# Kernel optimization log

Hardware: AMD Instinct MI355X
Metric: run time of the kernel (lower is better)

The kernel has to match this reference:

```python
import jax, jax.numpy as jnp
import numpy as np

DIM = 96
HEADS = 3
RES = (128, 128)
KH, KW = 8, 8
SH, SW = 4, 4  # window_size // 2, shift enabled
N = KH * KW
EPS_LN = 1e-5


def _rel_tables():
    # relative coords table fed to CPB-MLP, shape [(2KH-1)*(2KW-1), 2]
    ch = np.arange(-(KH - 1), KH, dtype=np.float32)
    cw = np.arange(-(KW - 1), KW, dtype=np.float32)
    t = np.stack(np.meshgrid(ch, cw, indexing='ij'), axis=-1)
    t[..., 0] /= (KH - 1)
    t[..., 1] /= (KW - 1)
    t *= 8.0
    t = np.sign(t) * np.log2(np.abs(t) + 1.0) / np.log2(8.0)
    # relative position index, shape [N, N]
    coords = np.stack(np.meshgrid(np.arange(KH), np.arange(KW), indexing='ij'))
    cf = coords.reshape(2, -1)
    rel = (cf[:, :, None] - cf[:, None, :]).transpose(1, 2, 0)
    rel[..., 0] += KH - 1
    rel[..., 1] += KW - 1
    rel[..., 0] *= 2 * KW - 1
    idx = rel.sum(-1)
    return jnp.asarray(t.reshape(-1, 2)), jnp.asarray(idx)


def _attn_mask():
    # shifted-window attention mask, shape [nW, N, N]
    H, W = RES
    img = np.zeros((H, W), np.float32)
    cnt = 0
    for hs in (slice(0, -KH), slice(-KH, -SH), slice(-SH, None)):
        for ws in (slice(0, -KW), slice(-KW, -SW), slice(-SW, None)):
            img[hs, ws] = cnt
            cnt += 1
    mw = img.reshape(H // KH, KH, W // KW, KW).transpose(0, 2, 1, 3).reshape(-1, N)
    am = mw[:, None, :] - mw[:, :, None]
    am = np.where(am != 0, -100.0, 0.0).astype(np.float32)
    return jnp.asarray(am)


_CPB_TABLE, _REL_IDX = _rel_tables()
_ATTN_MASK = _attn_mask()


def _layernorm(x, w, b):
    mu = x.mean(-1, keepdims=True)
    var = x.var(-1, keepdims=True)
    return (x - mu) / jnp.sqrt(var + EPS_LN) * w + b


def setup_inputs() -> dict:
    key = jax.random.key(0)
    ks = jax.random.split(key, 16)
    B = 32
    H, W = RES
    hid = 4 * DIM
    s = 0.02
    return {
        'x': jax.random.normal(ks[0], (B, H * W, DIM), jnp.float32),
        'norm1_w': jnp.ones((DIM,), jnp.float32),
        'norm1_b': jnp.zeros((DIM,), jnp.float32),
        'qkv_w': jax.random.normal(ks[1], (3 * DIM, DIM), jnp.float32) * s,
        'q_bias': jnp.zeros((DIM,), jnp.float32),
        'v_bias': jnp.zeros((DIM,), jnp.float32),
        'logit_scale': jnp.full((HEADS, 1, 1), np.log(10.0), jnp.float32),
        'cpb_w1': jax.random.normal(ks[2], (512, 2), jnp.float32) * s,
        'cpb_b1': jnp.zeros((512,), jnp.float32),
        'cpb_w2': jax.random.normal(ks[3], (HEADS, 512), jnp.float32) * s,
        'proj_w': jax.random.normal(ks[4], (DIM, DIM), jnp.float32) * s,
        'proj_b': jnp.zeros((DIM,), jnp.float32),
        'norm2_w': jnp.ones((DIM,), jnp.float32),
        'norm2_b': jnp.zeros((DIM,), jnp.float32),
        'mlp_w1': jax.random.normal(ks[5], (hid, DIM), jnp.float32) * s,
        'mlp_b1': jnp.zeros((hid,), jnp.float32),
        'mlp_w2': jax.random.normal(ks[6], (DIM, hid), jnp.float32) * s,
        'mlp_b2': jnp.zeros((DIM,), jnp.float32),
    }


def reference(x, norm1_w, norm1_b, qkv_w, q_bias, v_bias, logit_scale,
              cpb_w1, cpb_b1, cpb_w2, proj_w, proj_b,
              norm2_w, norm2_b, mlp_w1, mlp_b1, mlp_w2, mlp_b2):
    B, L, C = x.shape
    H, W = RES
    hd = C // HEADS
    shortcut = x

    # cyclic shift + window partition: [B*nW, N, C]
    xi = jnp.roll(x.reshape(B, H, W, C), (-SH, -SW), axis=(1, 2))
    xw = xi.reshape(B, H // KH, KH, W // KW, KW, C).transpose(0, 1, 3, 2, 4, 5)
    xw = xw.reshape(-1, N, C)
    B_ = xw.shape[0]

    # qkv with zero k-bias
    qkv_b = jnp.concatenate([q_bias, jnp.zeros_like(v_bias), v_bias])
    qkv = (xw @ qkv_w.T + qkv_b).reshape(B_, N, 3, HEADS, hd).transpose(2, 0, 3, 1, 4)
    q, k, v = qkv[0], qkv[1], qkv[2]

    # cosine attention with clamped learned logit scale
    qn = q / jnp.maximum(jnp.linalg.norm(q, axis=-1, keepdims=True), 1e-12)
    kn = k / jnp.maximum(jnp.linalg.norm(k, axis=-1, keepdims=True), 1e-12)
    attn = jnp.einsum('bhnd,bhmd->bhnm', qn, kn)
    ls = jnp.exp(jnp.minimum(logit_scale, jnp.log(100.0)))
    attn = attn * ls

    # CPB-MLP relative position bias, gathered into [heads, N, N]
    bias_t = jax.nn.relu(_CPB_TABLE @ cpb_w1.T + cpb_b1) @ cpb_w2.T
    rpb = 16.0 * jax.nn.sigmoid(bias_t[_REL_IDX]).transpose(2, 0, 1)
    attn = attn + rpb[None]

    # shift mask, then softmax
    nW = _ATTN_MASK.shape[0]
    attn = attn.reshape(B_ // nW, nW, HEADS, N, N) + _ATTN_MASK[None, :, None]
    attn = jax.nn.softmax(attn.reshape(B_, HEADS, N, N), axis=-1)

    out = jnp.einsum('bhnm,bhmd->bhnd', attn, v).transpose(0, 2, 1, 3).reshape(B_, N, C)
    out = out @ proj_w.T + proj_b

    # window reverse + reverse shift
    out = out.reshape(B, H // KH, W // KW, KH, KW, C).transpose(0, 1, 3, 2, 4, 5)
    out = out.reshape(B, H, W, C)
    out = jnp.roll(out, (SH, SW), axis=(1, 2)).reshape(B, L, C)

    # SwinV2 post-norm residuals
    x = shortcut + _layernorm(out, norm1_w, norm1_b)
    h = jax.nn.gelu(x @ mlp_w1.T + mlp_b1, approximate=False) @ mlp_w2.T + mlp_b2
    x = x + _layernorm(h, norm2_w, norm2_b)
    return x
```

## Files before the change

kernel.cpp:

```cpp
#include <hip/hip_runtime.h>
#include <math.h>


constexpr int WIN=8, CD=96, RH=128, RW=128, SHF=4;

constexpr int KN_S=40, VT_S=72, WB_S=104;
constexpr int OFF_KN=0;
constexpr int OFF_VT=2560;
constexpr int PAN_SH=10240;
constexpr int OFF_WB0=4864;
constexpr int OFF_WB1=15104;
constexpr int LDS_SHORTS=25344;
constexpr int LDS_BYTES = LDS_SHORTS*2;

typedef float f32x4 __attribute__((ext_vector_type(4)));
typedef short s16x8 __attribute__((ext_vector_type(8)));
typedef short s16x4 __attribute__((ext_vector_type(4)));
typedef int   i32x2 __attribute__((ext_vector_type(2)));
typedef int   i32x4 __attribute__((ext_vector_type(4)));
typedef unsigned int u32x2 __attribute__((ext_vector_type(2)));

#define MFMA16(a,b,c) __builtin_amdgcn_mfma_f32_16x16x32_bf16((a),(b),(c),0,0,0)

#if __has_builtin(__builtin_amdgcn_permlane32_swap) && __has_builtin(__builtin_amdgcn_permlane16_swap)
#define HAVE_PLSWAP 1
#else
#define HAVE_PLSWAP 0
#endif

#define RAW_LDS_BARRIER() do { \
    asm volatile("s_waitcnt lgkmcnt(0)" ::: "memory"); \
    __builtin_amdgcn_s_barrier(); \
    asm volatile("" ::: "memory"); } while (0)

__device__ __forceinline__ short f2bf(float f) {
    __bf16 b = (__bf16)f;
    return __builtin_bit_cast(short, b);
}
__device__ __forceinline__ s16x8 ld8(const short* p) {
    return *reinterpret_cast<const s16x8*>(p);
}
__device__ __forceinline__ s16x4 pack4(float a, float b, float c, float d) {
    s16x4 r; r[0]=f2bf(a); r[1]=f2bf(b); r[2]=f2bf(c); r[3]=f2bf(d);
    return r;
}
__device__ __forceinline__ s16x8 abf_from_f32(const float* p) {
    const f32x4* q = reinterpret_cast<const f32x4*>(p);
    f32x4 a = q[0], b = q[1];
    s16x8 r;
    r[0]=f2bf(a[0]); r[1]=f2bf(a[1]); r[2]=f2bf(a[2]); r[3]=f2bf(a[3]);
    r[4]=f2bf(b[0]); r[5]=f2bf(b[1]); r[6]=f2bf(b[2]); r[7]=f2bf(b[3]);
    return r;
}

#if HAVE_PLSWAP
__device__ __forceinline__ void plswap32(unsigned &a, unsigned &b) {
    u32x2 r = __builtin_amdgcn_permlane32_swap(a, b, false, false);
    a = r[0]; b = r[1];
}
__device__ __forceinline__ void plswap16(unsigned &a, unsigned &b) {
    u32x2 r = __builtin_amdgcn_permlane16_swap(a, b, false, false);
    a = r[0]; b = r[1];
}
#endif

__device__ __forceinline__ s16x8 xposeT(s16x4 p0, s16x4 p1, int l) {
    i32x2 q0 = __builtin_bit_cast(i32x2, p0);
    i32x2 q1 = __builtin_bit_cast(i32x2, p1);
#if HAVE_PLSWAP
    (void)l;
    unsigned a0 = (unsigned)q0[0], a1 = (unsigned)q0[1];
    unsigned b0 = (unsigned)q1[0], b1 = (unsigned)q1[1];
    plswap32(a0, b0);
    plswap32(a1, b1);
    plswap16(a0, b0);
    plswap16(a1, b1);
    i32x4 w; w[0]=(int)a0; w[1]=(int)a1; w[2]=(int)b0; w[3]=(int)b1;
    return __builtin_bit_cast(s16x8, w);
#else
    const int l15 = l & 15, lg = l >> 4;
    const int L1 = l15 + (((2*lg  )&3)<<4);
    const int L2 = l15 + (((2*lg+1)&3)<<4);
    const bool lo = (lg & 2) == 0;
    int a0 = __shfl(q0[0], L1), b0 = __shfl(q1[0], L1);
    int a1 = __shfl(q0[1], L1), b1 = __shfl(q1[1], L1);
    int a2 = __shfl(q0[0], L2), b2 = __shfl(q1[0], L2);
    int a3 = __shfl(q0[1], L2), b3 = __shfl(q1[1], L2);
    i32x4 w;
    w[0] = lo ? a0 : b0;
    w[1] = lo ? a1 : b1;
    w[2] = lo ? a2 : b2;
    w[3] = lo ? a3 : b3;
    return __builtin_bit_cast(s16x8, w);
#endif
}
__device__ __forceinline__ float xsum4(float v) {
#if HAVE_PLSWAP
    unsigned a = __builtin_bit_cast(unsigned, v), b = a;
    plswap16(a, b);
    float s = __builtin_bit_cast(float, a) + __builtin_bit_cast(float, b);
    unsigned c = __builtin_bit_cast(unsigned, s), d = c;
    plswap32(c, d);
    return __builtin_bit_cast(float, c) + __builtin_bit_cast(float, d);
#else
    v += __shfl_xor(v,16); v += __shfl_xor(v,32); return v;
#endif
}
__device__ __forceinline__ float xmax4(float v) {
#if HAVE_PLSWAP
    unsigned a = __builtin_bit_cast(unsigned, v), b = a;
    plswap16(a, b);
    float s = fmaxf(__builtin_bit_cast(float, a), __builtin_bit_cast(float, b));
    unsigned c = __builtin_bit_cast(unsigned, s), d = c;
    plswap32(c, d);
    return fmaxf(__builtin_bit_cast(float, c), __builtin_bit_cast(float, d));
#else
    v = fmaxf(v, __shfl_xor(v,16)); v = fmaxf(v, __shfl_xor(v,32)); return v;
#endif
}
__device__ __forceinline__ int region_id(int hh, int ww) {
    int rr = (hh < RH-WIN) ? 0 : ((hh < RH-SHF) ? 1 : 2);
    int rc = (ww < RW-WIN) ? 0 : ((ww < RW-SHF) ? 1 : 2);
    return rr*3 + rc;
}
__device__ __forceinline__ float gelu_f(float h) {
    float u = h * (1.5957691216f + 0.0713548163f * h * h);
    float e = __expf(-u);
    return h * __builtin_amdgcn_rcpf(1.f + e);
}

__device__ __forceinline__ void stage_panel(const short* __restrict__ pan,
                                            short* dst, int wv, int l) {
    const char* g = (const char*)pan + l*16;
    char* d = (char*)dst;
    #pragma unroll
    for (int k = 0; k < 5; ++k) {
        int i = wv + k*4;
        __builtin_amdgcn_global_load_lds(
            (const __attribute__((address_space(1))) unsigned int*)(g + i*1024),
            (__attribute__((address_space(3))) unsigned int*)(d + i*1024),
            16, 0, 0);
    }
}

__global__ __launch_bounds__(256) void cpb_kernel(
    const float* __restrict__ w1, const float* __restrict__ b1,
    const float* __restrict__ w2, float* __restrict__ rpb)
{
    int g = blockIdx.x*256 + threadIdx.x;
    if (g >= 225*3) return;
    int e = g/3, h = g - e*3;
    int a = e/15, bb = e - a*15;
    float z0 = (float)(a-7) * (8.0f/7.0f);
    float z1 = (float)(bb-7) * (8.0f/7.0f);
    float s0 = (z0>0.f)?1.f:((z0<0.f)?-1.f:0.f);
    float s1 = (z1>0.f)?1.f:((z1<0.f)?-1.f:0.f);
    float t0 = s0 * log2f(fabsf(z0)+1.f) * (1.f/3.f);
    float t1 = s1 * log2f(fabsf(z1)+1.f) * (1.f/3.f);
    float acc = 0.f;
    for (int k = 0; k < 512; ++k) {
        float hv = t0*w1[2*k] + t1*w1[2*k+1] + b1[k];
        hv = fmaxf(hv, 0.f);
        acc += hv * w2[h*512 + k];
    }
    rpb[g] = 16.f / (1.f + __expf(-acc));
}

__global__ __launch_bounds__(256) void biasbuild_kernel(
    const float* __restrict__ rpb, float* __restrict__ biasT)
{
    int g = blockIdx.x*256 + threadIdx.x;
    if (g >= 3*64*64) return;
    int h = g >> 12, rem = g & 4095, i = rem >> 6, j = rem & 63;
    int ih = i>>3, iw = i&7, jh = j>>3, jw = j&7;
    int idx = (ih-jh+7)*15 + (iw-jw+7);
    biasT[g] = rpb[idx*3 + h];
}

__global__ __launch_bounds__(256) void wcvt_kernel(
    const float* __restrict__ qkvw, const float* __restrict__ projw,
    const float* __restrict__ w1,   const float* __restrict__ w2,
    short* __restrict__ wpan)
{
    int i = blockIdx.x*256 + threadIdx.x;
    if (i >= 12*9216) return;
    int p = i / 9216;
    int rem = i - p*9216;
    int r = rem / 96;
    int col = rem - r*96;
    float v;
    if (p < 3)        v = qkvw[((r>>5)*96 + p*32 + (r&31))*96 + col];
    else if (p == 3)  v = projw[r*96 + col];
    else if (((p-4)&1) == 0) { int c = (p-4)>>1; v = w1[(c*96 + r)*96 + col]; }
    else              { int c = (p-4)>>1; v = w2[r*384 + c*96 + col]; }
    wpan[p*PAN_SH + r*WB_S + col] = f2bf(v);
}

__global__ __launch_bounds__(256,3) void fused_kernel(
    const float* __restrict__ x,
    const float* __restrict__ n1w, const float* __restrict__ n1b,
    const float* __restrict__ qb,  const float* __restrict__ vb,
    const float* __restrict__ lgs, const float* __restrict__ pb,
    const float* __restrict__ n2w, const float* __restrict__ n2b,
    const float* __restrict__ b1,  const float* __restrict__ b2,
    const float* __restrict__ biasT,
    const short* __restrict__ wpan,
    float* __restrict__ out)
{
    extern __shared__ __align__(16) short smem[];
    short* kn  = smem + OFF_KN;
    short* vt  = smem + OFF_VT;
    short* wb0 = smem + OFF_WB0;
    short* wb1 = smem + OFF_WB1;

    const int t = threadIdx.x;
    const int l = t & 63;
    const int wv = t >> 6;
    const int l15 = l & 15;
    const int lg  = l >> 4;

    const int wid = blockIdx.x;
    const int b = wid >> 8, wi = wid & 255, wh = wi >> 4, ww = wi & 15;
    const float* xb = x + (size_t)b * (RH*RW*CD);

    const int arow = wv*16 + l15;
    const int ahs = (wh*WIN + (arow>>3) + SHF) & (RH-1);
    const int aws = (ww*WIN + (arow&7)  + SHF) & (RW-1);
    const unsigned go = ((unsigned)(b << 14) + ahs*RW + aws) * CD;
    const float* xrow = xb + (ahs*RW + aws)*CD;
    s16x8 xa[3];
    #pragma unroll
    for (int kt = 0; kt < 3; ++kt) xa[kt] = abf_from_f32(xrow + kt*32 + lg*8);

    f32x4 maskv[4];
    {
        int regi = region_id(wh*WIN + (arow>>3), ww*WIN + (arow&7));
        #pragma unroll
        for (int mt = 0; mt < 4; ++mt)
            #pragma unroll
            for (int rr = 0; rr < 4; ++rr) {
                int j = mt*16 + lg*4 + rr;
                int regj = region_id(wh*WIN + (j>>3), ww*WIN + (j&7));
                maskv[mt][rr] = (regi != regj) ? -100.f : 0.f;
            }
    }

    stage_panel(wpan, wb0, wv, l);

    s16x4 aop[6];

    #pragma unroll
    for (int h = 0; h < 3; ++h) {
        __syncthreads();
        stage_panel(wpan + (h+1)*PAN_SH, (h&1) ? wb0 : wb1, wv, l);
        const short* wbuf = (h&1) ? wb1 : wb0;

        const float ls = __expf(fminf(lgs[h], 4.60517019f));

        f32x4 qbf[2], vbf[2];
        #pragma unroll
        for (int nt = 0; nt < 2; ++nt) {
            qbf[nt] = *reinterpret_cast<const f32x4*>(qb + h*32 + nt*16 + lg*4);
            vbf[nt] = *reinterpret_cast<const f32x4*>(vb + h*32 + nt*16 + lg*4);
        }

        f32x4 qc[2], kc[2], vc[2];
        #pragma unroll
        for (int sec = 0; sec < 3; ++sec) {
            #pragma unroll
            for (int nt = 0; nt < 2; ++nt) {
                f32x4 c = (sec==0) ? qbf[nt]
                        : (sec==2) ? vbf[nt] : (f32x4){0.f,0.f,0.f,0.f};
                const short* wp = wbuf + (sec*32 + nt*16 + l15)*WB_S;
                #pragma unroll
                for (int kt = 0; kt < 3; ++kt)
                    c = MFMA16(ld8(wp + kt*32 + lg*8), xa[kt], c);
                if (sec==0) qc[nt]=c; else if (sec==1) kc[nt]=c; else vc[nt]=c;
            }
        }
        float sq = ((qc[0][0]*qc[0][0] + qc[0][1]*qc[0][1])
                  + (qc[0][2]*qc[0][2] + qc[0][3]*qc[0][3]))
                 + ((qc[1][0]*qc[1][0] + qc[1][1]*qc[1][1])
                  + (qc[1][2]*qc[1][2] + qc[1][3]*qc[1][3]));
        float sk = ((kc[0][0]*kc[0][0] + kc[0][1]*kc[0][1])
                  + (kc[0][2]*kc[0][2] + kc[0][3]*kc[0][3]))
                 + ((kc[1][0]*kc[1][0] + kc[1][1]*kc[1][1])
                  + (kc[1][2]*kc[1][2] + kc[1][3]*kc[1][3]));
        sq = xsum4(sq);
        sk = xsum4(sk);
        float scq = ls * __builtin_amdgcn_rsqf(fmaxf(sq, 1e-24f));
        float sck =      __builtin_amdgcn_rsqf(fmaxf(sk, 1e-24f));

        s16x4 qp0 = pack4(qc[0][0]*scq, qc[0][1]*scq, qc[0][2]*scq, qc[0][3]*scq);
        s16x4 qp1 = pack4(qc[1][0]*scq, qc[1][1]*scq, qc[1][2]*scq, qc[1][3]*scq);
        #pragma unroll
        for (int nt = 0; nt < 2; ++nt) {
            *reinterpret_cast<s16x4*>(kn + arow*KN_S + nt*16 + lg*4) =
                pack4(kc[nt][0]*sck, kc[nt][1]*sck, kc[nt][2]*sck, kc[nt][3]*sck);
            #pragma unroll
            for (int rr = 0; rr < 4; ++rr)
                vt[(nt*16 + lg*4 + rr)*VT_S + arow] = f2bf(vc[nt][rr]);
        }
        RAW_LDS_BARRIER();

        f32x4 bvm[4];
        const float* bh = biasT + h*4096 + arow*64;
        #pragma unroll
        for (int mt = 0; mt < 4; ++mt) {
            f32x4 bv = *reinterpret_cast<const f32x4*>(bh + mt*16 + lg*4);
            #pragma unroll
            for (int rr = 0; rr < 4; ++rr) bvm[mt][rr] = bv[rr] + maskv[mt][rr];
        }

        s16x8 qA = xposeT(qp0, qp1, l);
        f32x4 st[4];
        #pragma unroll
        for (int mt = 0; mt < 4; ++mt)
            st[mt] = MFMA16(ld8(kn + (mt*16 + l15)*KN_S + lg*8), qA, bvm[mt]);

        float m0 = fmaxf(fmaxf(st[0][0],st[0][1]), fmaxf(st[0][2],st[0][3]));
        float m1 = fmaxf(fmaxf(st[1][0],st[1][1]), fmaxf(st[1][2],st[1][3]));
        float m2 = fmaxf(fmaxf(st[2][0],st[2][1]), fmaxf(st[2][2],st[2][3]));
        float m3 = fmaxf(fmaxf(st[3][0],st[3][1]), fmaxf(st[3][2],st[3][3]));
        float mx = xmax4(fmaxf(fmaxf(m0,m1), fmaxf(m2,m3)));
        float sp[4];
        #pragma unroll
        for (int mt = 0; mt < 4; ++mt) {
            #pragma unroll
            for (int rr = 0; rr < 4; ++rr)
                st[mt][rr] = __expf(st[mt][rr] - mx);
            sp[mt] = (st[mt][0] + st[mt][1]) + (st[mt][2] + st[mt][3]);
        }
        float sm = xsum4((sp[0] + sp[1]) + (sp[2] + sp[3]));
        float inv = __builtin_amdgcn_rcpf(sm);

        s16x4 pw[4];
        #pragma unroll
        for (int mt = 0; mt < 4; ++mt)
            pw[mt] = pack4(st[mt][0], st[mt][1], st[mt][2], st[mt][3]);

        s16x8 pB0 = xposeT(pw[0], pw[1], l);
        s16x8 pB1 = xposeT(pw[2], pw[3], l);
        #pragma unroll
        for (int nt2 = 0; nt2 < 2; ++nt2) {
            f32x4 o = {0.f,0.f,0.f,0.f};
            o = MFMA16(ld8(vt + (nt2*16+l15)*VT_S + 0  + lg*8), pB0, o);
            o = MFMA16(ld8(vt + (nt2*16+l15)*VT_S + 32 + lg*8), pB1, o);
            aop[h*2 + nt2] = pack4(o[0]*inv, o[1]*inv, o[2]*inv, o[3]*inv);
        }
    }

    stage_panel(wpan + 4*PAN_SH, wb0, wv, l);

    s16x8 aB[3];
    #pragma unroll
    for (int kt = 0; kt < 3; ++kt)
        aB[kt] = xposeT(aop[2*kt], aop[2*kt+1], l);
    f32x4 pc[6];
    #pragma unroll
    for (int nt = 0; nt < 6; ++nt) {
        f32x4 c = *reinterpret_cast<const f32x4*>(pb + nt*16 + lg*4);
        const short* wp = wb1 + (nt*16 + l15)*WB_S;
        #pragma unroll
        for (int kt = 0; kt < 3; ++kt)
            c = MFMA16(ld8(wp + kt*32 + lg*8), aB[kt], c);
        pc[nt] = c;
    }

    f32x4 x1v[6];
    s16x4 x1p[6];
    {
        float sA=0.f, sB=0.f, s2A=0.f, s2B=0.f;
        #pragma unroll
        for (int nt = 0; nt < 6; ++nt) {
            f32x4 v = pc[nt];
            float ps  = (v[0]+v[1]) + (v[2]+v[3]);
            float ps2 = (v[0]*v[0]+v[1]*v[1]) + (v[2]*v[2]+v[3]*v[3]);
            if (nt & 1) { sB += ps; s2B += ps2; } else { sA += ps; s2A += ps2; }
        }
        float s = xsum4(sA + sB), s2 = xsum4(s2A + s2B);
        float mu  = s * (1.f/96.f);
        float var = s2 * (1.f/96.f) - mu*mu;
        float rstd = __builtin_amdgcn_rsqf(var + 1e-5f);
        #pragma unroll
        for (int nt = 0; nt < 6; ++nt) {
            f32x4 w1f = *reinterpret_cast<const f32x4*>(n1w + nt*16 + lg*4);
            f32x4 b1f = *reinterpret_cast<const f32x4*>(n1b + nt*16 + lg*4);
            f32x4 xv  = *reinterpret_cast<const f32x4*>(x + go + nt*16 + lg*4);
            f32x4 v;
            #pragma unroll
            for (int rr = 0; rr < 4; ++rr)
                v[rr] = xv[rr] + (pc[nt][rr] - mu)*rstd*w1f[rr] + b1f[rr];
            x1v[nt] = v;
            x1p[nt] = pack4(v[0], v[1], v[2], v[3]);
        }
    }

    s16x8 x1B[3];
    #pragma unroll
    for (int kt = 0; kt < 3; ++kt)
        x1B[kt] = xposeT(x1p[2*kt], x1p[2*kt+1], l);

    f32x4 oa[6];
    #pragma unroll
    for (int nt = 0; nt < 6; ++nt)
        oa[nt] = *reinterpret_cast<const f32x4*>(b2 + nt*16 + lg*4);

    for (int c = 0; c < 4; ++c) {
        __syncthreads();
        stage_panel(wpan + (5+2*c)*PAN_SH, wb1, wv, l);
        s16x4 hp[6];
        #pragma unroll
        for (int nt = 0; nt < 6; ++nt) {
            f32x4 a = *reinterpret_cast<const f32x4*>(b1 + c*96 + nt*16 + lg*4);
            const short* wp = wb0 + (nt*16 + l15)*WB_S;
            #pragma unroll
            for (int kt = 0; kt < 3; ++kt)
                a = MFMA16(ld8(wp + kt*32 + lg*8), x1B[kt], a);
            hp[nt] = pack4(gelu_f(a[0]), gelu_f(a[1]), gelu_f(a[2]), gelu_f(a[3]));
        }
        __syncthreads();
        if (c < 3) stage_panel(wpan + (6+2*c)*PAN_SH, wb0, wv, l);
        s16x8 hB[3];
        #pragma unroll
        for (int kt = 0; kt < 3; ++kt)
            hB[kt] = xposeT(hp[2*kt], hp[2*kt+1], l);
        #pragma unroll
        for (int nt = 0; nt < 6; ++nt) {
            const short* wp = wb1 + (nt*16 + l15)*WB_S;
            #pragma unroll
            for (int kt = 0; kt < 3; ++kt)
                oa[nt] = MFMA16(ld8(wp + kt*32 + lg*8), hB[kt], oa[nt]);
        }
    }

    {
        float sA=0.f, sB=0.f, s2A=0.f, s2B=0.f;
        #pragma unroll
        for (int nt = 0; nt < 6; ++nt) {
            f32x4 v = oa[nt];
            float ps  = (v[0]+v[1]) + (v[2]+v[3]);
            float ps2 = (v[0]*v[0]+v[1]*v[1]) + (v[2]*v[2]+v[3]*v[3]);
            if (nt & 1) { sB += ps; s2B += ps2; } else { sA += ps; s2A += ps2; }
        }
        float s = xsum4(sA + sB), s2 = xsum4(s2A + s2B);
        float mu  = s * (1.f/96.f);
        float var = s2 * (1.f/96.f) - mu*mu;
        float rstd = __builtin_amdgcn_rsqf(var + 1e-5f);
        #pragma unroll
        for (int nt = 0; nt < 6; ++nt) {
            f32x4 w2f = *reinterpret_cast<const f32x4*>(n2w + nt*16 + lg*4);
            f32x4 bb2 = *reinterpret_cast<const f32x4*>(n2b + nt*16 + lg*4);
            f32x4 res;
            #pragma unroll
            for (int rr = 0; rr < 4; ++rr)
                res[rr] = x1v[nt][rr] + (oa[nt][rr] - mu)*rstd*w2f[rr] + bb2[rr];
            *reinterpret_cast<f32x4*>(out + go + nt*16 + lg*4) = res;
        }
    }
}

extern "C" void kernel_launch(void* const* d_in, const int* in_sizes, int n_in,
                              void* d_out, int out_size, void* d_ws, size_t ws_size,
                              hipStream_t stream) {
    const float* x       = (const float*)d_in[0];
    const float* norm1_w = (const float*)d_in[1];
    const float* norm1_b = (const float*)d_in[2];
    const float* qkv_w   = (const float*)d_in[3];
    const float* q_bias  = (const float*)d_in[4];
    const float* v_bias  = (const float*)d_in[5];
    const float* lgs     = (const float*)d_in[6];
    const float* cpb_w1  = (const float*)d_in[7];
    const float* cpb_b1  = (const float*)d_in[8];
    const float* cpb_w2  = (const float*)d_in[9];
    const float* proj_w  = (const float*)d_in[10];
    const float* proj_b  = (const float*)d_in[11];
    const float* norm2_w = (const float*)d_in[12];
    const float* norm2_b = (const float*)d_in[13];
    const float* mlp_w1  = (const float*)d_in[14];
    const float* mlp_b1  = (const float*)d_in[15];
    const float* mlp_w2  = (const float*)d_in[16];
    const float* mlp_b2  = (const float*)d_in[17];

    char* wsb = (char*)d_ws;
    float* rpbTab = (float*)wsb;
    float* biasT  = (float*)(wsb + 4096);
    short* wpan   = (short*)(wsb + 53248);

    float* out = (float*)d_out;

    hipFuncSetAttribute(reinterpret_cast<const void*>(fused_kernel),
                        hipFuncAttributeMaxDynamicSharedMemorySize, LDS_BYTES);

    cpb_kernel<<<3, 256, 0, stream>>>(cpb_w1, cpb_b1, cpb_w2, rpbTab);
    biasbuild_kernel<<<48, 256, 0, stream>>>(rpbTab, biasT);
    wcvt_kernel<<<432, 256, 0, stream>>>(qkv_w, proj_w, mlp_w1, mlp_w2, wpan);
    fused_kernel<<<8192, 256, LDS_BYTES, stream>>>(x, norm1_w, norm1_b,
                                                   q_bias, v_bias, lgs, proj_b,
                                                   norm2_w, norm2_b, mlp_b1, mlp_b2,
                                                   biasT, wpan, out);
}
```

Measured before the change: 376.7 us.

## Software-pipeline next head's QKV projection under current head's softmax

Restructures the per-head attention loop so the QKV MFMA projection for head h+1 is issued right after the score MFMAs of head h. It then overlaps with that head's softmax and PV work. Both first weight panels are staged up front, and panel staging shifts one head ahead. The K/V LDS writes for the next head move behind a barrier at the end of each iteration. The aim is to hide MFMA and LDS latency in the dependent softmax chain, at the cost of more live registers, which may lower occupancy or cause spills.

```diff
diff --git a/kernel.cpp b/kernel.cpp
--- a/kernel.cpp
+++ b/kernel.cpp
@@ -245,32 +245,16 @@
             }
     }
 
-    stage_panel(wpan, wb0, wv, l);
-
-    s16x4 aop[6];
-
-    #pragma unroll
-    for (int h = 0; h < 3; ++h) {
-        __syncthreads();
-        stage_panel(wpan + (h+1)*PAN_SH, (h&1) ? wb0 : wb1, wv, l);
-        const short* wbuf = (h&1) ? wb1 : wb0;
-
-        const float ls = __expf(fminf(lgs[h], 4.60517019f));
-
-        f32x4 qbf[2], vbf[2];
-        #pragma unroll
-        for (int nt = 0; nt < 2; ++nt) {
-            qbf[nt] = *reinterpret_cast<const f32x4*>(qb + h*32 + nt*16 + lg*4);
-            vbf[nt] = *reinterpret_cast<const f32x4*>(vb + h*32 + nt*16 + lg*4);
-        }
-
-        f32x4 qc[2], kc[2], vc[2];
+    auto qkv_compute = [&](const short* wbuf, int hh,
+                           f32x4 qc[2], f32x4 kc[2], f32x4 vc[2]) {
         #pragma unroll
         for (int sec = 0; sec < 3; ++sec) {
             #pragma unroll
             for (int nt = 0; nt < 2; ++nt) {
-                f32x4 c = (sec==0) ? qbf[nt]
-                        : (sec==2) ? vbf[nt] : (f32x4){0.f,0.f,0.f,0.f};
+                f32x4 c;
+                if (sec==0)      c = *reinterpret_cast<const f32x4*>(qb + hh*32 + nt*16 + lg*4);
+                else if (sec==2) c = *reinterpret_cast<const f32x4*>(vb + hh*32 + nt*16 + lg*4);
+                else             c = (f32x4){0.f,0.f,0.f,0.f};
                 const short* wp = wbuf + (sec*32 + nt*16 + l15)*WB_S;
                 #pragma unroll
                 for (int kt = 0; kt < 3; ++kt)
@@ -278,6 +262,9 @@
                 if (sec==0) qc[nt]=c; else if (sec==1) kc[nt]=c; else vc[nt]=c;
             }
         }
+    };
+    auto qk_norms = [&](const f32x4 qc[2], const f32x4 kc[2], int hh,
+                        float &scq, float &sck) {
         float sq = ((qc[0][0]*qc[0][0] + qc[0][1]*qc[0][1])
                   + (qc[0][2]*qc[0][2] + qc[0][3]*qc[0][3]))
                  + ((qc[1][0]*qc[1][0] + qc[1][1]*qc[1][1])
@@ -288,11 +275,23 @@
                   + (kc[1][2]*kc[1][2] + kc[1][3]*kc[1][3]));
         sq = xsum4(sq);
         sk = xsum4(sk);
-        float scq = ls * __builtin_amdgcn_rsqf(fmaxf(sq, 1e-24f));
-        float sck =      __builtin_amdgcn_rsqf(fmaxf(sk, 1e-24f));
-
-        s16x4 qp0 = pack4(qc[0][0]*scq, qc[0][1]*scq, qc[0][2]*scq, qc[0][3]*scq);
-        s16x4 qp1 = pack4(qc[1][0]*scq, qc[1][1]*scq, qc[1][2]*scq, qc[1][3]*scq);
+        float ls = __expf(fminf(lgs[hh], 4.60517019f));
+        scq = ls * __builtin_amdgcn_rsqf(fmaxf(sq, 1e-24f));
+        sck =      __builtin_amdgcn_rsqf(fmaxf(sk, 1e-24f));
+    };
+
+    stage_panel(wpan,          wb0, wv, l);
+    stage_panel(wpan + PAN_SH, wb1, wv, l);
+    __syncthreads();
+
+    s16x4 qp0, qp1;
+    {
+        f32x4 qc[2], kc[2], vc[2];
+        qkv_compute(wb0, 0, qc, kc, vc);
+        float scq, sck;
+        qk_norms(qc, kc, 0, scq, sck);
+        qp0 = pack4(qc[0][0]*scq, qc[0][1]*scq, qc[0][2]*scq, qc[0][3]*scq);
+        qp1 = pack4(qc[1][0]*scq, qc[1][1]*scq, qc[1][2]*scq, qc[1][3]*scq);
         #pragma unroll
         for (int nt = 0; nt < 2; ++nt) {
             *reinterpret_cast<s16x4*>(kn + arow*KN_S + nt*16 + lg*4) =
@@ -301,7 +300,14 @@
             for (int rr = 0; rr < 4; ++rr)
                 vt[(nt*16 + lg*4 + rr)*VT_S + arow] = f2bf(vc[nt][rr]);
         }
-        RAW_LDS_BARRIER();
+    }
+    RAW_LDS_BARRIER();
+
+    s16x4 aop[6];
+
+    #pragma unroll
+    for (int h = 0; h < 3; ++h) {
+        stage_panel(wpan + (h+2)*PAN_SH, (h&1) ? wb1 : wb0, wv, l);
 
         f32x4 bvm[4];
         const float* bh = biasT + h*4096 + arow*64;
@@ -317,6 +323,10 @@
         #pragma unroll
         for (int mt = 0; mt < 4; ++mt)
             st[mt] = MFMA16(ld8(kn + (mt*16 + l15)*KN_S + lg*8), qA, bvm[mt]);
+
+        f32x4 nqc[2], nkc[2], nvc[2];
+        if (h < 2)
+            qkv_compute((h&1) ? wb0 : wb1, h+1, nqc, nkc, nvc);
 
         float m0 = fmaxf(fmaxf(st[0][0],st[0][1]), fmaxf(st[0][2],st[0][3]));
         float m1 = fmaxf(fmaxf(st[1][0],st[1][1]), fmaxf(st[1][2],st[1][3]));
@@ -348,9 +358,26 @@
             o = MFMA16(ld8(vt + (nt2*16+l15)*VT_S + 32 + lg*8), pB1, o);
             aop[h*2 + nt2] = pack4(o[0]*inv, o[1]*inv, o[2]*inv, o[3]*inv);
         }
-    }
-
-    stage_panel(wpan + 4*PAN_SH, wb0, wv, l);
+
+        if (h < 2) {
+            float scq, sck;
+            qk_norms(nqc, nkc, h+1, scq, sck);
+            s16x4 nq0 = pack4(nqc[0][0]*scq, nqc[0][1]*scq, nqc[0][2]*scq, nqc[0][3]*scq);
+            s16x4 nq1 = pack4(nqc[1][0]*scq, nqc[1][1]*scq, nqc[1][2]*scq, nqc[1][3]*scq);
+            __syncthreads();
+            #pragma unroll
+            for (int nt = 0; nt < 2; ++nt) {
+                *reinterpret_cast<s16x4*>(kn + arow*KN_S + nt*16 + lg*4) =
+                    pack4(nkc[nt][0]*sck, nkc[nt][1]*sck,
+                          nkc[nt][2]*sck, nkc[nt][3]*sck);
+                #pragma unroll
+                for (int rr = 0; rr < 4; ++rr)
+                    vt[(nt*16 + lg*4 + rr)*VT_S + arow] = f2bf(nvc[nt][rr]);
+            }
+            RAW_LDS_BARRIER();
+            qp0 = nq0; qp1 = nq1;
+        }
+    }
 
     s16x8 aB[3];
     #pragma unroll
```

Result: faster. 355.3 us (-5.7%).
